# Optimization experiments

Hardware: AMD Instinct MI355X
Metric: run time of the kernel (lower is better)

The kernel has to match this reference:

```python
import jax, jax.numpy as jnp
import numpy as np

C = 128          # num_channels
S = 3000         # sequence_num
INTER = 30
EXTRACT = S // INTER  # 100
EPS = 1e-5


def _layernorm(y, g, b):
    # LayerNorm over last (channel) axis, eps=1e-5 like torch default
    m = jnp.mean(y, axis=-1, keepdims=True)
    v = jnp.mean(jnp.square(y - m), axis=-1, keepdims=True)
    return (y - m) * jax.lax.rsqrt(v + EPS) * g + b


def setup_inputs() -> dict:
    key = jax.random.key(0)
    ks = jax.random.split(key, 4)
    x = jax.random.normal(ks[0], (32, 4, C, S), dtype=jnp.float32)
    # xavier_normal Linear weights, zero bias; LayerNorm gamma=1, beta=0
    std = float(np.sqrt(2.0 / (C + C)))
    def lin_w(k):
        return jax.random.normal(k, (C, C), dtype=jnp.float32) * std
    Wq = lin_w(ks[1]); Wk = lin_w(ks[2]); Wp = lin_w(ks[3])
    z = jnp.zeros((C,), jnp.float32); o = jnp.ones((C,), jnp.float32)
    return {
        "x": x,
        "Wq": Wq, "bq": z, "gq": o, "betaq": z,
        "Wk": Wk, "bk": z, "gk": o, "betak": z,
        "Wp": Wp, "bp": z, "gp": o, "betap": z,
    }


def reference(x, Wq, bq, gq, betaq, Wk, bk, gk, betak, Wp, bp, gp, betap):
    # x: [b, o, c, s]
    temp = jnp.swapaxes(x, -1, -2)                         # [b,o,s,c]
    q = _layernorm(temp @ Wq.T + bq, gq, betaq)            # [b,o,s,c]
    k = _layernorm(temp @ Wk.T + bk, gk, betak)            # [b,o,s,c]
    q = jnp.swapaxes(q, -1, -2)                            # [b,o,c,s]
    k = jnp.swapaxes(k, -1, -2)                            # [b,o,c,s]
    scaling = jnp.asarray(EXTRACT, x.dtype) ** 0.5         # sqrt(extract_sequence)
    atten = jnp.einsum('bocs,boms->bocm', q, k) / scaling  # [b,o,c,c]
    score = jax.nn.softmax(atten, axis=-1)                 # [b,o,c,c]
    # faithful to source: contracts m (score rows sum to 1)
    out = jnp.einsum('bocs,bocm->bocs', x, score)          # [b,o,c,s]
    out = jnp.swapaxes(out, -1, -2)                        # [b,o,s,c]
    out = _layernorm(out @ Wp.T + bp, gp, betap)
    return jnp.swapaxes(out, -1, -2)                       # [b,o,c,s]
```

## Files before the change

### kernel.cpp

```cpp
#include <hip/hip_runtime.h>
#include <hip/hip_bf16.h>


#define C    128
#define SEQ  3000
#define NG   128
#define NT   128
#define NBLK ((SEQ + NT - 1) / NT)

typedef float f4 __attribute__((ext_vector_type(4)));
typedef short short8 __attribute__((ext_vector_type(8)));

__device__ __forceinline__ unsigned short f2bf(float f) {
    union { float f; unsigned u; } v; v.f = f;
    unsigned r = v.u + 0x7fffu + ((v.u >> 16) & 1u);
    return (unsigned short)(r >> 16);
}

__device__ __forceinline__ int swz(int row, int chunk) {
    return chunk ^ ((row ^ (row >> 2)) & 15);
}

__global__ void cvt_wp(const float* __restrict__ Wp, unsigned short* __restrict__ out) {
    int i = blockIdx.x * 256 + threadIdx.x;
    if (i < C * C) out[i] = f2bf(Wp[i]);
}

__global__ __launch_bounds__(256, 2) void gemm_ln_mfma(
    const float* __restrict__ x,
    const unsigned short* __restrict__ wbf,
    const float* __restrict__ bp,
    const float* __restrict__ gp,
    const float* __restrict__ bep,
    float* __restrict__ out)
{
    __shared__ __align__(16) unsigned short Wl[C * C];
    __shared__ __align__(16) unsigned short Xl[NT * C];

    const int g  = blockIdx.y;
    const int s0 = blockIdx.x * NT;
    const float* xg = x + (size_t)g * (C * SEQ);
    float* og = out + (size_t)g * (C * SEQ);
    const int t = threadIdx.x;

    {
        const uint4* wsrc = (const uint4*)wbf;
        #pragma unroll
        for (int i = 0; i < 8; ++i) {
            int cid = t + 256 * i;
            int c  = cid >> 4;
            int ch = cid & 15;
            uint4 v = wsrc[cid];
            *(uint4*)&Wl[c * C + swz(c, ch) * 8] = v;
        }
    }

    {
        const int sq  = t & 31;
        const int mcb = t >> 5;
        const int s_loc  = 4 * sq;
        const int s_glob = s0 + s_loc;
        const bool valid = (s_glob + 3) < SEQ;
        #pragma unroll
        for (int half = 0; half < 2; ++half) {
            const int mc = mcb + 8 * half;
            f4 r[8];
            const float* xp = xg + (size_t)(mc * 8) * SEQ + s_glob;
            #pragma unroll
            for (int rr = 0; rr < 8; ++rr) {
                if (valid) r[rr] = *(const f4*)(xp + (size_t)rr * SEQ);
                else       r[rr] = (f4){0.f, 0.f, 0.f, 0.f};
            }
            #pragma unroll
            for (int j = 0; j < 4; ++j) {
                const int sl = s_loc + j;
                uint4 pk;
                pk.x = (unsigned)f2bf(r[0][j]) | ((unsigned)f2bf(r[1][j]) << 16);
                pk.y = (unsigned)f2bf(r[2][j]) | ((unsigned)f2bf(r[3][j]) << 16);
                pk.z = (unsigned)f2bf(r[4][j]) | ((unsigned)f2bf(r[5][j]) << 16);
                pk.w = (unsigned)f2bf(r[6][j]) | ((unsigned)f2bf(r[7][j]) << 16);
                *(uint4*)&Xl[sl * C + swz(sl, mc) * 8] = pk;
            }
        }
    }
    __syncthreads();

    const int w    = t >> 6;
    const int lane = t & 63;
    const int col  = lane & 15;
    const int quad = lane >> 4;

    f4 acc[2][8];
    #pragma unroll
    for (int nt = 0; nt < 2; ++nt)
        #pragma unroll
        for (int mt = 0; mt < 8; ++mt) acc[nt][mt] = (f4){0.f, 0.f, 0.f, 0.f};

    #pragma unroll
    for (int kc = 0; kc < 4; ++kc) {
        short8 a[8], b[2];
        #pragma unroll
        for (int mt = 0; mt < 8; ++mt) {
            const int row = 16 * mt + col;
            a[mt] = *(const short8*)&Wl[row * C + swz(row, 4 * kc + quad) * 8];
        }
        #pragma unroll
        for (int nt = 0; nt < 2; ++nt) {
            const int srow = 32 * w + 16 * nt + col;
            b[nt] = *(const short8*)&Xl[srow * C + swz(srow, 4 * kc + quad) * 8];
        }
        #pragma unroll
        for (int nt = 0; nt < 2; ++nt)
            #pragma unroll
            for (int mt = 0; mt < 8; ++mt)
                acc[nt][mt] = __builtin_amdgcn_mfma_f32_16x16x32_bf16(
                    a[mt], b[nt], acc[nt][mt], 0, 0, 0);
    }

    #pragma unroll
    for (int mt = 0; mt < 8; ++mt) {
        const f4 b4 = *(const f4*)(bp + 16 * mt + 4 * quad);
        #pragma unroll
        for (int nt = 0; nt < 2; ++nt)
            #pragma unroll
            for (int r = 0; r < 4; ++r) acc[nt][mt][r] += b4[r];
    }

    float mean[2], rstd[2];
    #pragma unroll
    for (int nt = 0; nt < 2; ++nt) {
        float s = 0.f, q = 0.f;
        #pragma unroll
        for (int mt = 0; mt < 8; ++mt)
            #pragma unroll
            for (int r = 0; r < 4; ++r) {
                float y = acc[nt][mt][r];
                s += y; q += y * y;
            }
        s += __shfl_xor(s, 16); q += __shfl_xor(q, 16);
        s += __shfl_xor(s, 32); q += __shfl_xor(q, 32);
        float m = s * (1.0f / C);
        float v = q * (1.0f / C) - m * m;
        mean[nt] = m;
        rstd[nt] = rsqrtf(v + 1e-5f);
    }

    #pragma unroll
    for (int mt = 0; mt < 8; ++mt) {
        const f4 g4 = *(const f4*)(gp  + 16 * mt + 4 * quad);
        const f4 e4 = *(const f4*)(bep + 16 * mt + 4 * quad);
        #pragma unroll
        for (int nt = 0; nt < 2; ++nt) {
            const int sg = s0 + 32 * w + 16 * nt + col;
            if (sg < SEQ) {
                #pragma unroll
                for (int r = 0; r < 4; ++r) {
                    const int c = 16 * mt + 4 * quad + r;
                    og[(size_t)c * SEQ + sg] =
                        (acc[nt][mt][r] - mean[nt]) * rstd[nt] * g4[r] + e4[r];
                }
            }
        }
    }
}

extern "C" void kernel_launch(void* const* d_in, const int* in_sizes, int n_in,
                              void* d_out, int out_size, void* d_ws, size_t ws_size,
                              hipStream_t stream) {
    const float* x   = (const float*)d_in[0];
    const float* Wp  = (const float*)d_in[9];
    const float* bp  = (const float*)d_in[10];
    const float* gp  = (const float*)d_in[11];
    const float* bep = (const float*)d_in[12];
    float* out = (float*)d_out;
    unsigned short* wbf = (unsigned short*)d_ws;

    hipLaunchKernelGGL(cvt_wp, dim3(64), dim3(256), 0, stream, Wp, wbf);

    dim3 grid(NBLK, NG);
    hipLaunchKernelGGL(gemm_ln_mfma, grid, dim3(256), 0, stream,
                       x, wbf, bp, gp, bep, out);
}
```

Baseline: 398.4 us.

## Halve sequence tile, read bf16 weights from global, raise occupancy

Cuts the per-block sequence tile from 128 to 64 columns and drops the shared-memory copy of the weight matrix. MFMA A-fragments are now loaded straight from global/L2, and each wave keeps its X fragments in registers for all k-chunks. The smaller LDS footprint and fewer accumulators allow four blocks per CU and give more blocks to hide memory latency. It also switches to the packed hardware bf16 conversion and relaxes the tail validity check. The trade-off is repeated global loads of weights per block instead of reuse from LDS.

```diff
diff --git a/kernel.cpp b/kernel.cpp
--- a/kernel.cpp
+++ b/kernel.cpp
@@ -5,7 +5,7 @@
 #define C    128
 #define SEQ  3000
 #define NG   128
-#define NT   128
+#define NT   64
 #define NBLK ((SEQ + NT - 1) / NT)
 
 typedef float f4 __attribute__((ext_vector_type(4)));
@@ -17,6 +17,12 @@
     return (unsigned short)(r >> 16);
 }
 
+__device__ __forceinline__ unsigned pk2bf(float lo, float hi) {
+    __hip_bfloat162 h = __float22bfloat162_rn(float2{lo, hi});
+    union { __hip_bfloat162 h; unsigned u; } v; v.h = h;
+    return v.u;
+}
+
 __device__ __forceinline__ int swz(int row, int chunk) {
     return chunk ^ ((row ^ (row >> 2)) & 15);
 }
@@ -26,7 +32,7 @@
     if (i < C * C) out[i] = f2bf(Wp[i]);
 }
 
-__global__ __launch_bounds__(256, 2) void gemm_ln_mfma(
+__global__ __launch_bounds__(256, 4) void gemm_ln_mfma(
     const float* __restrict__ x,
     const unsigned short* __restrict__ wbf,
     const float* __restrict__ bp,
@@ -34,7 +40,6 @@
     const float* __restrict__ bep,
     float* __restrict__ out)
 {
-    __shared__ __align__(16) unsigned short Wl[C * C];
     __shared__ __align__(16) unsigned short Xl[NT * C];
 
     const int g  = blockIdx.y;
@@ -44,43 +49,27 @@
     const int t = threadIdx.x;
 
     {
-        const uint4* wsrc = (const uint4*)wbf;
-        #pragma unroll
-        for (int i = 0; i < 8; ++i) {
-            int cid = t + 256 * i;
-            int c  = cid >> 4;
-            int ch = cid & 15;
-            uint4 v = wsrc[cid];
-            *(uint4*)&Wl[c * C + swz(c, ch) * 8] = v;
-        }
-    }
-
-    {
-        const int sq  = t & 31;
-        const int mcb = t >> 5;
+        const int sq  = t & 15;
+        const int mc  = t >> 4;
         const int s_loc  = 4 * sq;
         const int s_glob = s0 + s_loc;
-        const bool valid = (s_glob + 3) < SEQ;
+        const bool valid = s_glob < SEQ;
+        f4 r[8];
+        const float* xp = xg + (size_t)(mc * 8) * SEQ + s_glob;
         #pragma unroll
-        for (int half = 0; half < 2; ++half) {
-            const int mc = mcb + 8 * half;
-            f4 r[8];
-            const float* xp = xg + (size_t)(mc * 8) * SEQ + s_glob;
-            #pragma unroll
-            for (int rr = 0; rr < 8; ++rr) {
-                if (valid) r[rr] = *(const f4*)(xp + (size_t)rr * SEQ);
-                else       r[rr] = (f4){0.f, 0.f, 0.f, 0.f};
-            }
-            #pragma unroll
-            for (int j = 0; j < 4; ++j) {
-                const int sl = s_loc + j;
-                uint4 pk;
-                pk.x = (unsigned)f2bf(r[0][j]) | ((unsigned)f2bf(r[1][j]) << 16);
-                pk.y = (unsigned)f2bf(r[2][j]) | ((unsigned)f2bf(r[3][j]) << 16);
-                pk.z = (unsigned)f2bf(r[4][j]) | ((unsigned)f2bf(r[5][j]) << 16);
-                pk.w = (unsigned)f2bf(r[6][j]) | ((unsigned)f2bf(r[7][j]) << 16);
-                *(uint4*)&Xl[sl * C + swz(sl, mc) * 8] = pk;
-            }
+        for (int rr = 0; rr < 8; ++rr) {
+            if (valid) r[rr] = *(const f4*)(xp + (size_t)rr * SEQ);
+            else       r[rr] = (f4){0.f, 0.f, 0.f, 0.f};
+        }
+        #pragma unroll
+        for (int j = 0; j < 4; ++j) {
+            const int sl = s_loc + j;
+            uint4 pk;
+            pk.x = pk2bf(r[0][j], r[1][j]);
+            pk.y = pk2bf(r[2][j], r[3][j]);
+            pk.z = pk2bf(r[4][j], r[5][j]);
+            pk.w = pk2bf(r[6][j], r[7][j]);
+            *(uint4*)&Xl[sl * C + swz(sl, mc) * 8] = pk;
         }
     }
     __syncthreads();
@@ -90,75 +79,56 @@
     const int col  = lane & 15;
     const int quad = lane >> 4;
 
-    f4 acc[2][8];
+    short8 b[4];
+    {
+        const int srow = 16 * w + col;
+        #pragma unroll
+        for (int kc = 0; kc < 4; ++kc)
+            b[kc] = *(const short8*)&Xl[srow * C + swz(srow, 4 * kc + quad) * 8];
+    }
+
+    f4 acc[8];
     #pragma unroll
-    for (int nt = 0; nt < 2; ++nt)
-        #pragma unroll
-        for (int mt = 0; mt < 8; ++mt) acc[nt][mt] = (f4){0.f, 0.f, 0.f, 0.f};
+    for (int mt = 0; mt < 8; ++mt) acc[mt] = (f4){0.f, 0.f, 0.f, 0.f};
 
     #pragma unroll
     for (int kc = 0; kc < 4; ++kc) {
-        short8 a[8], b[2];
+        short8 a[8];
         #pragma unroll
-        for (int mt = 0; mt < 8; ++mt) {
-            const int row = 16 * mt + col;
-            a[mt] = *(const short8*)&Wl[row * C + swz(row, 4 * kc + quad) * 8];
-        }
+        for (int mt = 0; mt < 8; ++mt)
+            a[mt] = *(const short8*)(wbf + (16 * mt + col) * C + (4 * kc + quad) * 8);
         #pragma unroll
-        for (int nt = 0; nt < 2; ++nt) {
-            const int srow = 32 * w + 16 * nt + col;
-            b[nt] = *(const short8*)&Xl[srow * C + swz(srow, 4 * kc + quad) * 8];
-        }
-        #pragma unroll
-        for (int nt = 0; nt < 2; ++nt)
-            #pragma unroll
-            for (int mt = 0; mt < 8; ++mt)
-                acc[nt][mt] = __builtin_amdgcn_mfma_f32_16x16x32_bf16(
-                    a[mt], b[nt], acc[nt][mt], 0, 0, 0);
+        for (int mt = 0; mt < 8; ++mt)
+            acc[mt] = __builtin_amdgcn_mfma_f32_16x16x32_bf16(a[mt], b[kc], acc[mt], 0, 0, 0);
     }
 
+    float s = 0.f, q = 0.f;
     #pragma unroll
     for (int mt = 0; mt < 8; ++mt) {
         const f4 b4 = *(const f4*)(bp + 16 * mt + 4 * quad);
         #pragma unroll
-        for (int nt = 0; nt < 2; ++nt)
-            #pragma unroll
-            for (int r = 0; r < 4; ++r) acc[nt][mt][r] += b4[r];
+        for (int r = 0; r < 4; ++r) {
+            float y = acc[mt][r] + b4[r];
+            acc[mt][r] = y;
+            s += y; q += y * y;
+        }
     }
+    s += __shfl_xor(s, 16); q += __shfl_xor(q, 16);
+    s += __shfl_xor(s, 32); q += __shfl_xor(q, 32);
+    const float mean = s * (1.0f / C);
+    const float var  = q * (1.0f / C) - mean * mean;
+    const float rstd = rsqrtf(var + 1e-5f);
 
-    float mean[2], rstd[2];
-    #pragma unroll
-    for (int nt = 0; nt < 2; ++nt) {
-        float s = 0.f, q = 0.f;
+    const int sg = s0 + 16 * w + col;
+    if (sg < SEQ) {
         #pragma unroll
-        for (int mt = 0; mt < 8; ++mt)
+        for (int mt = 0; mt < 8; ++mt) {
+            const f4 g4 = *(const f4*)(gp  + 16 * mt + 4 * quad);
+            const f4 e4 = *(const f4*)(bep + 16 * mt + 4 * quad);
             #pragma unroll
             for (int r = 0; r < 4; ++r) {
-                float y = acc[nt][mt][r];
-                s += y; q += y * y;
-            }
-        s += __shfl_xor(s, 16); q += __shfl_xor(q, 16);
-        s += __shfl_xor(s, 32); q += __shfl_xor(q, 32);
-        float m = s * (1.0f / C);
-        float v = q * (1.0f / C) - m * m;
-        mean[nt] = m;
-        rstd[nt] = rsqrtf(v + 1e-5f);
-    }
-
-    #pragma unroll
-    for (int mt = 0; mt < 8; ++mt) {
-        const f4 g4 = *(const f4*)(gp  + 16 * mt + 4 * quad);
-        const f4 e4 = *(const f4*)(bep + 16 * mt + 4 * quad);
-        #pragma unroll
-        for (int nt = 0; nt < 2; ++nt) {
-            const int sg = s0 + 32 * w + 16 * nt + col;
-            if (sg < SEQ) {
-                #pragma unroll
-                for (int r = 0; r < 4; ++r) {
-                    const int c = 16 * mt + 4 * quad + r;
-                    og[(size_t)c * SEQ + sg] =
-                        (acc[nt][mt][r] - mean[nt]) * rstd[nt] * g4[r] + e4[r];
-                }
+                const int c = 16 * mt + 4 * quad + r;
+                og[(size_t)c * SEQ + sg] = (acc[mt][r] - mean) * rstd * g4[r] + e4[r];
             }
         }
     }
```

New measurement: 1.088 ms. +173.1%, slower.
